# Kernel tuning notes

Measured on AMD Instinct MI355X. Metric: run time of the kernel, lower is better.

The kernel has to match this reference:

```python
import jax, jax.numpy as jnp
import numpy as np

WEIGHT = 1.0  # init kwarg: loss weight
N = 4096
D_FEAT = 128


def _pairwise_dist(x):
    # x: [n, d] -> D: [n, n] Euclidean distances (safe sqrt for grad at 0)
    sq = jnp.sum(x * x, axis=-1)
    d2 = sq[:, None] + sq[None, :] - 2.0 * (x @ x.T)
    d2 = jnp.maximum(d2, 0.0)
    pos = d2 > 1e-12
    return jnp.where(pos, jnp.sqrt(jnp.where(pos, d2, 1.0)), 0.0)


def _prim_mst(D):
    # Vectorized Prim: returns (parents, children) of the n-1 MST edges.
    # filtration value (VR complex truncated at max_dimension=1).
    n = D.shape[0]
    INF = jnp.finfo(D.dtype).max
    visited0 = jnp.zeros(n, dtype=bool).at[0].set(True)
    mind0 = D[0]
    parent0 = jnp.zeros(n, dtype=jnp.int32)

    def step(carry, _):
        visited, mind, parent = carry
        j = jnp.argmin(jnp.where(visited, INF, mind))
        pj = parent[j]
        visited = visited.at[j].set(True)
        better = (D[j] < mind) & (~visited)
        mind = jnp.where(better, D[j], mind)
        parent = jnp.where(better, j, parent)
        return (visited, mind, parent), (pj, j.astype(jnp.int32))

    _, (pjs, js) = jax.lax.scan(step, (visited0, mind0, parent0), None, length=n - 1)
    return pjs, js


def _h1_persistence(x):
    # H1 diagram for VR complex with max_dimension=1: a 1-cycle is born when a
    # non-MST edge appears; with no 2-simplices it never dies, so deaths are
    # capped at the maximal filtration value. Persistence = cap - birth.
    n = x.shape[0]
    D = _pairwise_dist(x)
    pjs, js = _prim_mst(D)
    tree = jnp.zeros((n, n), dtype=bool)
    tree = tree.at[pjs, js].set(True)
    tree = tree | tree.T
    iu = np.triu_indices(n, 1)  # static indices
    births = D[iu]              # [n*(n-1)/2]
    is_tree = tree[iu]
    cap = jnp.max(D)
    # tree edges are H0 (not H1): give them zero persistence (diagonal points)
    return jnp.where(is_tree, 0.0, cap - births)


def _wasserstein_1d(p1, p2):
    # 1-Wasserstein between equal-size persistence multisets via sorted matching
    # (deaths share a common cap per diagram, so matching by sorted persistence).
    return jnp.sum(jnp.abs(jnp.sort(p1) - jnp.sort(p2)))


def setup_inputs() -> dict:
    key = jax.random.key(0)
    k1, k2, k3, k4 = jax.random.split(key, 4)
    return {
        "graph1_features": jax.random.normal(k1, (N, D_FEAT), dtype=jnp.float32),
        "graph1_edges": jax.random.randint(k2, (2, 8 * N), 0, N, dtype=jnp.int64),
        "graph2_features": jax.random.normal(k3, (N, D_FEAT), dtype=jnp.float32),
        "graph2_edges": jax.random.randint(k4, (2, 8 * N), 0, N, dtype=jnp.int64),
    }


def reference(graph1_features, graph1_edges, graph2_features, graph2_edges):
    # edge tensors are unused: the torch forward builds VR complexes from the
    # point clouds only (build_from_points), matching the original module.
    p1 = _h1_persistence(graph1_features)
    p2 = _h1_persistence(graph2_features)
    return WEIGHT * _wasserstein_1d(p1, p2)
```

## Files before the change

### kernel.cpp

```cpp
#include <hip/hip_runtime.h>
#include <stdint.h>

#define NN 4096
#define DF 128
#define NBINS 16384
#define NSLAB 256
#define BORUVKA_ROUNDS 12

typedef __attribute__((ext_vector_type(8))) short short8;
typedef __attribute__((ext_vector_type(4))) float floatx4;
typedef __attribute__((ext_vector_type(4))) unsigned short ushort4_t;
typedef __attribute__((ext_vector_type(8))) unsigned short ushort8_t;
typedef __attribute__((ext_vector_type(4))) int int4_t;
typedef __attribute__((ext_vector_type(2))) unsigned uvec2;

__device__ __forceinline__ unsigned bin_of(float v, float scale) {
  if (v < 0.f) v = 0.f;
  unsigned b = (unsigned)(v * scale);
  return b >= (unsigned)NBINS ? (unsigned)(NBINS - 1) : b;
}

__device__ __forceinline__ void gload16(const unsigned short* g, unsigned short* l) {
  __builtin_amdgcn_global_load_lds(
      (const __attribute__((address_space(1))) void*)g,
      (__attribute__((address_space(3))) void*)l, 16, 0, 0);
}

__global__ void k_rownorm(const float* __restrict__ x1, const float* __restrict__ x2,
                          float* __restrict__ sq) {
  int i = blockIdx.x * blockDim.x + threadIdx.x;
  if (i >= 2 * NN) return;
  const float* x = (i < NN) ? x1 : x2;
  int r = i & (NN - 1);
  const float* row = x + (size_t)r * DF;
  float s = 0.f;
  for (int k = 0; k < DF; ++k) s += row[k] * row[k];
  sq[i] = s;
}

__global__ __launch_bounds__(256) void k_bound(const float* __restrict__ sq,
                                               float* __restrict__ hdrf) {
  int t = threadIdx.x;
  float m = 0.f;
  for (int i = t; i < 2 * NN; i += 256) m = fmaxf(m, sq[i]);
  for (int off = 32; off > 0; off >>= 1) m = fmaxf(m, __shfl_down(m, off, 64));
  __shared__ float wm[4];
  if ((t & 63) == 0) wm[t >> 6] = m;
  __syncthreads();
  if (t == 0) {
    float mm = fmaxf(fmaxf(wm[0], wm[1]), fmaxf(wm[2], wm[3]));
    float dbound = 2.f * sqrtf(mm);
    hdrf[2] = 65535.f / dbound;
    hdrf[3] = dbound / 65535.f;
  }
}

__global__ void k_split(const float* __restrict__ x1, const float* __restrict__ x2,
                        unsigned short* __restrict__ xh, unsigned short* __restrict__ xl) {
  int i = blockIdx.x * blockDim.x + threadIdx.x;
  if (i >= 2 * NN * DF) return;
  const float* x = (i < NN * DF) ? x1 : x2;
  float v = x[i & (NN * DF - 1)];
  unsigned u = __float_as_uint(v);
  unsigned hu = u & 0xffff0000u;
  float hf = __uint_as_float(hu);
  float lf = v - hf;
  unsigned lu = __float_as_uint(lf) & 0xffff0000u;
  xh[i] = (unsigned short)(hu >> 16);
  xl[i] = (unsigned short)(lu >> 16);
}

__global__ void k_binit(int* __restrict__ comp, unsigned long long* __restrict__ compbest,
                        unsigned long long* __restrict__ bestkey,
                        int* __restrict__ mstcnt, int* __restrict__ ncomp) {
  int i = blockIdx.x * blockDim.x + threadIdx.x;
  if (i >= 2 * NN) return;
  comp[i] = i & (NN - 1);
  compbest[i] = ~0ull;
  bestkey[i] = ~0ull;
  if ((i & (NN - 1)) == 0) {
    mstcnt[i >> 12] = 0;
    ncomp[i >> 12] = NN;
  }
}

#define SJ 136
__global__ __launch_bounds__(256) void k_dist(const unsigned short* __restrict__ Xhi,
                                              const unsigned short* __restrict__ Xlo,
                                              const float* __restrict__ sq,
                                              const float* __restrict__ hdrf,
                                              unsigned short* __restrict__ Qbase,
                                              unsigned long long* __restrict__ bestkey_base,
                                              unsigned* __restrict__ caps) {
  int bi = blockIdx.y, bj = blockIdx.x;
  if (bi > bj) return;
  bool offdiag = (bi != bj);
  int g = blockIdx.z;
  const unsigned short* xh = Xhi + (size_t)g * NN * DF;
  const unsigned short* xl = Xlo + (size_t)g * NN * DF;
  const float* sqg = sq + g * NN;
  unsigned short* Q = Qbase + (size_t)g * NN * NN;
  float qs = hdrf[2];
  int t = threadIdx.x;
  int w = t >> 6, lane = t & 63;
  int m = lane & 15, quad = lane >> 4;
  int iw = (w >> 1) * 64, jw = (w & 1) * 64;
  int i0 = bi * 128 + iw;
  int j0 = bj * 128 + jw;

  __shared__ __align__(16) unsigned short SB[128 * SJ];

  int baseRow = (w < 2) ? bi * 128 : bj * 128;
  const unsigned short* src = (w == 0 || w == 2) ? xh : xl;
  unsigned short* ldsPiece = &SB[w * 4096];
  int rsub = lane >> 2;
  int kpart = (lane & 3) ^ ((lane >> 3) & 3);
  int fr = (quad ^ ((m >> 1) & 3)) << 3;

  floatx4 acc[4][4];
#pragma unroll
  for (int ti = 0; ti < 4; ++ti)
#pragma unroll
    for (int tj = 0; tj < 4; ++tj) acc[ti][tj] = (floatx4){0.f, 0.f, 0.f, 0.f};

  for (int s = 0; s < 4; ++s) {
    int kc = s * 32;
    if (s) __syncthreads();
#pragma unroll
    for (int i = 0; i < 8; ++i) {
      const unsigned short* gp =
          src + (size_t)(baseRow + i * 16 + rsub) * DF + kc + kpart * 8;
      gload16(gp, &ldsPiece[i * 512]);
    }
    __syncthreads();
    short8 ah[4], al[4], bh[4], bl[4];
#pragma unroll
    for (int ti = 0; ti < 4; ++ti) {
      int ra = (iw + ti * 16 + m) * 32 + fr;
      int rb = (jw + ti * 16 + m) * 32 + fr;
      ah[ti] = *(const short8*)&SB[ra];
      al[ti] = *(const short8*)&SB[4096 + ra];
      bh[ti] = *(const short8*)&SB[8192 + rb];
      bl[ti] = *(const short8*)&SB[12288 + rb];
    }
#pragma unroll
    for (int ti = 0; ti < 4; ++ti)
#pragma unroll
      for (int tj = 0; tj < 4; ++tj) {
        acc[ti][tj] = __builtin_amdgcn_mfma_f32_16x16x32_bf16(ah[ti], bh[tj], acc[ti][tj], 0, 0, 0);
        acc[ti][tj] = __builtin_amdgcn_mfma_f32_16x16x32_bf16(ah[ti], bl[tj], acc[ti][tj], 0, 0, 0);
        acc[ti][tj] = __builtin_amdgcn_mfma_f32_16x16x32_bf16(al[ti], bh[tj], acc[ti][tj], 0, 0, 0);
      }
  }

  float sqj[4];
#pragma unroll
  for (int tj = 0; tj < 4; ++tj) sqj[tj] = sqg[j0 + tj * 16 + m];
  float mx = 0.f;
  ushort4_t qv[4][4];
#pragma unroll
  for (int ti = 0; ti < 4; ++ti) {
    int ib = i0 + ti * 16 + quad * 4;
    float sqiv[4];
#pragma unroll
    for (int r = 0; r < 4; ++r) sqiv[r] = sqg[ib + r];
#pragma unroll
    for (int tj = 0; tj < 4; ++tj) {
#pragma unroll
      for (int r = 0; r < 4; ++r) {
        float d2 = sqiv[r] + sqj[tj] - 2.f * acc[ti][tj][r];
        d2 = fmaxf(d2, 0.f);
        float d = (d2 > 1e-12f) ? sqrtf(d2) : 0.f;
        mx = fmaxf(mx, d);
        unsigned q = (unsigned)(d * qs + 0.5f);
        if (q > 65535u) q = 65535u;
        qv[ti][tj][r] = (unsigned short)q;
      }
    }
  }

  __syncthreads();
  unsigned short* T = SB;
  int sub = t >> 4, l16 = t & 15;
  int l31 = lane & 31, half = lane >> 5;
  unsigned long long* bkp = bestkey_base + (size_t)g * NN;

  auto prefill_rows = [&](int rbase, int cbase, bool exdiag) {
#pragma unroll 4
    for (int ii = 0; ii < 16; ++ii) {
      int rr = w * 32 + ii * 2 + half;
      uvec2 vv = *(const uvec2*)&T[rr * SJ + l31 * 4];
      int row = rbase + rr;
      unsigned qq[4] = {vv[0] & 0xffffu, vv[0] >> 16, vv[1] & 0xffffu, vv[1] >> 16};
      unsigned kmin = 0xffffffffu;
#pragma unroll
      for (int u = 0; u < 4; ++u) {
        int cl = l31 * 4 + u;
        if (!exdiag || (cbase + cl) != row) {
          unsigned key = (qq[u] << 7) | (unsigned)cl;
          if (key < kmin) kmin = key;
        }
      }
#pragma unroll
      for (int off2 = 1; off2 < 32; off2 <<= 1) {
        unsigned o = (unsigned)__shfl_xor((int)kmin, off2, 32);
        if (o < kmin) kmin = o;
      }
      if (l31 == 0 && kmin != 0xffffffffu) {
        unsigned qk = kmin >> 7, cl = kmin & 127u;
        unsigned long long key64 = ((unsigned long long)qk << 24) |
                                   ((unsigned long long)row << 12) |
                                   (unsigned)(cbase + cl);
        atomicMin(&bkp[row], key64);
      }
    }
  };

#pragma unroll
  for (int ti = 0; ti < 4; ++ti) {
    int il = iw + ti * 16 + quad * 4;
#pragma unroll
    for (int tj = 0; tj < 4; ++tj) {
      int jl = jw + tj * 16 + m;
      *(ushort4_t*)&T[jl * SJ + il] = qv[ti][tj];
    }
  }
  __syncthreads();
#pragma unroll
  for (int k = 0; k < 8; ++k) {
    int jl = k * 16 + sub;
    int4_t v = *(const int4_t*)&T[jl * SJ + l16 * 8];
    *(int4_t*)&Q[(size_t)(bj * 128 + jl) * NN + bi * 128 + l16 * 8] = v;
  }
  prefill_rows(bj * 128, bi * 128, !offdiag);

  if (offdiag) {
    __syncthreads();
#pragma unroll
    for (int ti = 0; ti < 4; ++ti) {
      int il = iw + ti * 16 + quad * 4;
#pragma unroll
      for (int tj = 0; tj < 4; ++tj) {
        int jl = jw + tj * 16 + m;
#pragma unroll
        for (int r = 0; r < 4; ++r) T[(il + r) * SJ + jl] = qv[ti][tj][r];
      }
    }
    __syncthreads();
#pragma unroll
    for (int k = 0; k < 8; ++k) {
      int il = k * 16 + sub;
      int4_t v = *(const int4_t*)&T[il * SJ + l16 * 8];
      *(int4_t*)&Q[(size_t)(bi * 128 + il) * NN + bj * 128 + l16 * 8] = v;
    }
    prefill_rows(bi * 128, bj * 128, false);
  }

  for (int off = 32; off > 0; off >>= 1) mx = fmaxf(mx, __shfl_down(mx, off, 64));
  __shared__ float wmax[4];
  if (lane == 0) wmax[w] = mx;
  __syncthreads();
  if (t == 0) {
    float mm = fmaxf(fmaxf(wmax[0], wmax[1]), fmaxf(wmax[2], wmax[3]));
    atomicMax(&caps[g], __float_as_uint(mm));
  }
}

__global__ __launch_bounds__(256) void k_minedge(const unsigned short* __restrict__ Qbase,
                                                 const int* __restrict__ comp_base,
                                                 unsigned long long* __restrict__ compbest_base,
                                                 unsigned long long* __restrict__ bestkey_base,
                                                 const int* __restrict__ ncomp) {
  int g = blockIdx.y;
  if (ncomp[g] == 1) return;
  int w = threadIdx.x >> 6, lane = threadIdx.x & 63;
  int v = blockIdx.x * 4 + w;
  const int* comp = comp_base + g * NN;
  unsigned long long* cbest = compbest_base + (size_t)g * NN;
  unsigned long long* bkp = bestkey_base + (size_t)g * NN;
  int cv = comp[v];
  unsigned long long bk = bkp[v];
  if (bk != ~0ull) {
    int bj = (int)(bk & 0xfffull);
    if (comp[bj] != cv) {
      if (lane == 0) atomicMin(&cbest[cv], bk);
      return;
    }
  }
  const unsigned short* row = Qbase + ((size_t)g * NN + (size_t)v) * NN;
  unsigned best = 0xffffffffu;
#pragma unroll 4
  for (int it = 0; it < NN / 256; ++it) {
    int jb = (it * 64 + lane) * 4;
    ushort4_t rw = *(const ushort4_t*)&row[jb];
    int4_t cj = *(const int4_t*)&comp[jb];
#pragma unroll
    for (int u = 0; u < 4; ++u) {
      if (cj[u] != cv) {
        unsigned key = ((unsigned)rw[u] << 12) | (unsigned)(jb + u);
        if (key < best) best = key;
      }
    }
  }
  for (int off = 32; off > 0; off >>= 1) {
    unsigned o = (unsigned)__shfl_down((int)best, off, 64);
    if (o < best) best = o;
  }
  if (lane == 0) {
    unsigned long long b64 = ~0ull;
    if (best != 0xffffffffu)
      b64 = ((unsigned long long)(best >> 12) << 24) |
            ((unsigned long long)v << 12) | (best & 0xfffu);
    bkp[v] = b64;
    if (b64 != ~0ull) atomicMin(&cbest[cv], b64);
  }
}

__global__ __launch_bounds__(1024) void k_hook(unsigned long long* __restrict__ compbest_base,
                                               int* __restrict__ comp_base,
                                               const float* __restrict__ hdrf,
                                               float* __restrict__ mstw_base,
                                               int* __restrict__ mstcnt,
                                               int* __restrict__ ncomp) {
  int g = blockIdx.x;
  if (ncomp[g] == 1) return;
  unsigned long long* cb = compbest_base + (size_t)g * NN;
  int* comp = comp_base + g * NN;
  float* mstw = mstw_base + g * (NN - 1);
  float qinv = hdrf[3];
  __shared__ int par[NN];
  __shared__ unsigned char live[NN];
  __shared__ int newcnt;
  int t = threadIdx.x;
  if (t == 0) newcnt = 0;
  for (int c = t; c < NN; c += 1024) {
    unsigned long long key = cb[c];
    bool a = (key != ~0ull);
    live[c] = a ? 1 : 0;
    int p = c;
    if (a) {
      int j = (int)(key & 0xfffull);
      p = comp[j];
    }
    par[c] = p;
  }
  __syncthreads();
  for (int c = t; c < NN; c += 1024) {
    int p = par[c];
    if (p != c && par[p] == c && c < p) par[c] = c;
  }
  __syncthreads();
  for (int c = t; c < NN; c += 1024) {
    if (live[c] && par[c] != c) {
      float w = (float)((unsigned)(cb[c] >> 24)) * qinv;
      int slot = atomicAdd(&mstcnt[g], 1);
      mstw[slot] = w;
    }
  }
  __syncthreads();
  for (;;) {
    int np[NN / 1024];
    bool ch = false;
    int k = 0;
    for (int c = t; c < NN; c += 1024, ++k) {
      int p = par[c];
      int pp = par[p];
      np[k] = pp;
      if (pp != p) ch = true;
    }
    __syncthreads();
    k = 0;
    for (int c = t; c < NN; c += 1024, ++k) par[c] = np[k];
    if (!__syncthreads_or(ch)) break;
  }
  int cnt = 0;
  for (int c = t; c < NN; c += 1024)
    if (live[c] && par[c] == c) cnt++;
  for (int off = 32; off > 0; off >>= 1) cnt += __shfl_down(cnt, off, 64);
  if ((t & 63) == 0 && cnt) atomicAdd(&newcnt, cnt);
  for (int v = t; v < NN; v += 1024) comp[v] = par[comp[v]];
  for (int c = t; c < NN; c += 1024) cb[c] = ~0ull;
  __syncthreads();
  if (t == 0) ncomp[g] = newcnt;
}

__global__ __launch_bounds__(256) void k_hist(const unsigned short* __restrict__ Qbase,
                                              const unsigned* __restrict__ caps,
                                              const float* __restrict__ hdrf,
                                              unsigned* __restrict__ Hs) {
  __shared__ unsigned h[NBINS];
  int t = threadIdx.x;
  for (int i = t; i < NBINS; i += 256) h[i] = 0;
  int b = blockIdx.x;
  int g = b >> 8, s = b & (NSLAB - 1);
  const unsigned short* Q = Qbase + (size_t)g * NN * NN;
  float cap = __uint_as_float(caps[g]);
  float capmax = fmaxf(__uint_as_float(caps[0]), __uint_as_float(caps[1]));
  float scale = (float)NBINS / capmax;
  float qinv = hdrf[3];
  __syncthreads();
  for (int p = s; p < NN / 2; p += NSLAB) {
#pragma unroll
    for (int half = 0; half < 2; ++half) {
      int rrow = half ? (NN - 1 - p) : p;
      const unsigned short* row = Q + (size_t)rrow * NN;
      int j0 = rrow + 1;
      int ja = (j0 + 7) & ~7;
      if (t < ja - j0)
        atomicAdd(&h[bin_of(cap - (float)row[j0 + t] * qinv, scale)], 1u);
      int nch = (NN - ja) >> 3;
      for (int c = t; c < nch; c += 256) {
        ushort8_t v8 = *(const ushort8_t*)&row[ja + c * 8];
#pragma unroll
        for (int u = 0; u < 8; ++u)
          atomicAdd(&h[bin_of(cap - (float)v8[u] * qinv, scale)], 1u);
      }
    }
  }
  __syncthreads();
  unsigned* slab = Hs + (size_t)b * NBINS;
  for (int i = t; i < NBINS; i += 256) slab[i] = h[i];
}

__global__ void k_treefix(const float* __restrict__ twbase, const unsigned* __restrict__ caps,
                          unsigned* __restrict__ Hs) {
  int g = blockIdx.y;
  unsigned* hist = Hs + (size_t)(g * NSLAB) * NBINS;
  float cap = __uint_as_float(caps[g]);
  float capmax = fmaxf(__uint_as_float(caps[0]), __uint_as_float(caps[1]));
  float scale = (float)NBINS / capmax;
  int idx = blockIdx.x * blockDim.x + threadIdx.x;
  if (idx < NN - 1) {
    float w = twbase[g * (NN - 1) + idx];
    atomicSub(&hist[bin_of(cap - w, scale)], 1u);
    atomicAdd(&hist[0], 1u);
  }
}

__global__ __launch_bounds__(256) void k_merge(const unsigned* __restrict__ Hs,
                                               unsigned* __restrict__ Hm) {
  int id = blockIdx.x * 256 + threadIdx.x;
  int g = id >> 14;
  int i = id & (NBINS - 1);
  const unsigned* base = Hs + (size_t)(g * NSLAB) * NBINS + i;
  unsigned sum = 0;
  for (int s = 0; s < NSLAB; ++s) sum += base[(size_t)s * NBINS];
  Hm[id] = sum;
}

__global__ __launch_bounds__(256) void k_w1(const unsigned* __restrict__ Hm,
                                            const unsigned* __restrict__ caps,
                                            float* __restrict__ out) {
  int t = threadIdx.x;
  const int PB = NBINS / 256;
  int base = t * PB;
  long long tsum = 0;
  for (int i = 0; i < PB; ++i)
    tsum += (long long)(int)(Hm[base + i] - Hm[NBINS + base + i]);
  int lane = t & 63, wid = t >> 6;
  long long incl = tsum;
  for (int off = 1; off < 64; off <<= 1) {
    long long o = __shfl_up(incl, off, 64);
    if (lane >= off) incl += o;
  }
  __shared__ long long wtot[4];
  if (lane == 63) wtot[wid] = incl;
  __syncthreads();
  long long run = incl - tsum;
  for (int w = 0; w < wid; ++w) run += wtot[w];
  unsigned long long local = 0;
  for (int i = 0; i < PB; ++i) {
    run += (long long)(int)(Hm[base + i] - Hm[NBINS + base + i]);
    local += (unsigned long long)(run < 0 ? -run : run);
  }
  for (int off = 32; off > 0; off >>= 1) local += __shfl_down(local, off, 64);
  __shared__ unsigned long long wl[4];
  if (lane == 0) wl[wid] = local;
  __syncthreads();
  if (t == 0) {
    float capmax = fmaxf(__uint_as_float(caps[0]), __uint_as_float(caps[1]));
    double dt = (double)capmax / (double)NBINS;
    out[0] = (float)((double)(wl[0] + wl[1] + wl[2] + wl[3]) * dt);
  }
}

__global__ void k_fail(float* out) { out[0] = -1234567.0f; }

extern "C" void kernel_launch(void* const* d_in, const int* in_sizes, int n_in,
                              void* d_out, int out_size, void* d_ws, size_t ws_size,
                              hipStream_t stream) {
  const float* x1 = (const float*)d_in[0];
  const float* x2 = (const float*)d_in[2];
  float* out = (float*)d_out;
  char* ws = (char*)d_ws;

  const size_t offQ = 0;
  const size_t offS = 2ull * NN * NN * 2ull;
  const size_t offHm = offS + 2ull * NSLAB * NBINS * 4ull;
  const size_t offHdr = offHm + 2ull * NBINS * 4ull;
  const size_t offSq = offHdr + 64;
  const size_t offTw = offSq + 2ull * NN * 4ull;
  const size_t offCb = (offTw + 2ull * (NN - 1) * 4ull + 7ull) & ~7ull;
  const size_t offBk = offCb + 2ull * NN * 8ull;
  const size_t offCp = offBk + 2ull * NN * 8ull;
  const size_t offMeta = offCp + 2ull * NN * 4ull;
  const size_t needed = offMeta + 64;
  if (ws_size < needed) {
    hipLaunchKernelGGL(k_fail, dim3(1), dim3(1), 0, stream, out);
    return;
  }

  unsigned short* Qbase = (unsigned short*)(ws + offQ);
  unsigned* Hs = (unsigned*)(ws + offS);
  unsigned short* Xhi = (unsigned short*)(ws + offS);
  unsigned short* Xlo = (unsigned short*)(ws + offS + 2ull * NN * DF * 2ull);
  unsigned* Hm = (unsigned*)(ws + offHm);
  unsigned* caps = (unsigned*)(ws + offHdr);
  float* hdrf = (float*)(ws + offHdr);
  float* sq = (float*)(ws + offSq);
  float* tw = (float*)(ws + offTw);
  unsigned long long* compbest = (unsigned long long*)(ws + offCb);
  unsigned long long* bestkey = (unsigned long long*)(ws + offBk);
  int* comp = (int*)(ws + offCp);
  int* mstcnt = (int*)(ws + offMeta);
  int* ncomp = (int*)(ws + offMeta + 8);

  hipMemsetAsync(ws + offHdr, 0, 64, stream);

  hipLaunchKernelGGL(k_rownorm, dim3((2 * NN + 255) / 256), dim3(256), 0, stream, x1, x2, sq);
  hipLaunchKernelGGL(k_bound, dim3(1), dim3(256), 0, stream, sq, hdrf);
  hipLaunchKernelGGL(k_split, dim3((2 * NN * DF + 255) / 256), dim3(256), 0, stream,
                     x1, x2, Xhi, Xlo);
  hipLaunchKernelGGL(k_binit, dim3((2 * NN + 255) / 256), dim3(256), 0, stream,
                     comp, compbest, bestkey, mstcnt, ncomp);
  hipLaunchKernelGGL(k_dist, dim3(NN / 128, NN / 128, 2), dim3(256), 0, stream,
                     Xhi, Xlo, sq, hdrf, Qbase, bestkey, caps);
  for (int r = 0; r < BORUVKA_ROUNDS; ++r) {
    hipLaunchKernelGGL(k_minedge, dim3(NN / 4, 2), dim3(256), 0, stream,
                       Qbase, comp, compbest, bestkey, ncomp);
    hipLaunchKernelGGL(k_hook, dim3(2), dim3(1024), 0, stream,
                       compbest, comp, hdrf, tw, mstcnt, ncomp);
  }
  hipLaunchKernelGGL(k_hist, dim3(2 * NSLAB), dim3(256), 0, stream, Qbase, caps, hdrf, Hs);
  hipLaunchKernelGGL(k_treefix, dim3(16, 2), dim3(256), 0, stream, tw, caps, Hs);
  hipLaunchKernelGGL(k_merge, dim3(2 * NBINS / 256), dim3(256), 0, stream, Hs, Hm);
  hipLaunchKernelGGL(k_w1, dim3(1), dim3(256), 0, stream, Hm, caps, out);
}
```

Measured before the change: 354.3 us.

## Replace per-row best-edge cache with per-segment minima for Boruvka min-edge search

The distance kernel now stores, for each row, the minimum quantized key of each 128-column segment (32 per row) instead of a single atomic row minimum. The min-edge kernel reads these 32 segment minima, takes the best among segments whose argmin lies outside the vertex's component, and rescans only those segments whose cached minimum is smaller but falls inside the component. This is meant to avoid full 4096-column row rescans in later Boruvka rounds. In exchange it adds a 1 MB segmin buffer plus per-segment stores in k_dist, and uses a serial loop over flagged segments.

```diff
diff --git a/kernel.cpp b/kernel.cpp
--- a/kernel.cpp
+++ b/kernel.cpp
@@ -13,6 +13,7 @@
 typedef __attribute__((ext_vector_type(8))) unsigned short ushort8_t;
 typedef __attribute__((ext_vector_type(4))) int int4_t;
 typedef __attribute__((ext_vector_type(2))) unsigned uvec2;
+typedef __attribute__((ext_vector_type(2))) int ivec2;
 
 __device__ __forceinline__ unsigned bin_of(float v, float scale) {
   if (v < 0.f) v = 0.f;
@@ -71,13 +72,11 @@
 }
 
 __global__ void k_binit(int* __restrict__ comp, unsigned long long* __restrict__ compbest,
-                        unsigned long long* __restrict__ bestkey,
                         int* __restrict__ mstcnt, int* __restrict__ ncomp) {
   int i = blockIdx.x * blockDim.x + threadIdx.x;
   if (i >= 2 * NN) return;
   comp[i] = i & (NN - 1);
   compbest[i] = ~0ull;
-  bestkey[i] = ~0ull;
   if ((i & (NN - 1)) == 0) {
     mstcnt[i >> 12] = 0;
     ncomp[i >> 12] = NN;
@@ -90,7 +89,7 @@
                                               const float* __restrict__ sq,
                                               const float* __restrict__ hdrf,
                                               unsigned short* __restrict__ Qbase,
-                                              unsigned long long* __restrict__ bestkey_base,
+                                              unsigned* __restrict__ segmin_base,
                                               unsigned* __restrict__ caps) {
   int bi = blockIdx.y, bj = blockIdx.x;
   if (bi > bj) return;
@@ -100,6 +99,7 @@
   const unsigned short* xl = Xlo + (size_t)g * NN * DF;
   const float* sqg = sq + g * NN;
   unsigned short* Q = Qbase + (size_t)g * NN * NN;
+  unsigned* smg = segmin_base + (size_t)g * NN * 32;
   float qs = hdrf[2];
   int t = threadIdx.x;
   int w = t >> 6, lane = t & 63;
@@ -183,9 +183,8 @@
   unsigned short* T = SB;
   int sub = t >> 4, l16 = t & 15;
   int l31 = lane & 31, half = lane >> 5;
-  unsigned long long* bkp = bestkey_base + (size_t)g * NN;
-
-  auto prefill_rows = [&](int rbase, int cbase, bool exdiag) {
+
+  auto prefill_rows = [&](int rbase, int cbase, int segidx, bool exdiag) {
 #pragma unroll 4
     for (int ii = 0; ii < 16; ++ii) {
       int rr = w * 32 + ii * 2 + half;
@@ -206,13 +205,7 @@
         unsigned o = (unsigned)__shfl_xor((int)kmin, off2, 32);
         if (o < kmin) kmin = o;
       }
-      if (l31 == 0 && kmin != 0xffffffffu) {
-        unsigned qk = kmin >> 7, cl = kmin & 127u;
-        unsigned long long key64 = ((unsigned long long)qk << 24) |
-                                   ((unsigned long long)row << 12) |
-                                   (unsigned)(cbase + cl);
-        atomicMin(&bkp[row], key64);
-      }
+      if (l31 == 0) smg[(size_t)row * 32 + segidx] = kmin;
     }
   };
 
@@ -232,7 +225,7 @@
     int4_t v = *(const int4_t*)&T[jl * SJ + l16 * 8];
     *(int4_t*)&Q[(size_t)(bj * 128 + jl) * NN + bi * 128 + l16 * 8] = v;
   }
-  prefill_rows(bj * 128, bi * 128, !offdiag);
+  prefill_rows(bj * 128, bi * 128, bi, !offdiag);
 
   if (offdiag) {
     __syncthreads();
@@ -253,7 +246,7 @@
       int4_t v = *(const int4_t*)&T[il * SJ + l16 * 8];
       *(int4_t*)&Q[(size_t)(bi * 128 + il) * NN + bj * 128 + l16 * 8] = v;
     }
-    prefill_rows(bi * 128, bj * 128, false);
+    prefill_rows(bi * 128, bj * 128, bj, false);
   }
 
   for (int off = 32; off > 0; off >>= 1) mx = fmaxf(mx, __shfl_down(mx, off, 64));
@@ -267,9 +260,9 @@
 }
 
 __global__ __launch_bounds__(256) void k_minedge(const unsigned short* __restrict__ Qbase,
+                                                 const unsigned* __restrict__ segmin_base,
                                                  const int* __restrict__ comp_base,
                                                  unsigned long long* __restrict__ compbest_base,
-                                                 unsigned long long* __restrict__ bestkey_base,
                                                  const int* __restrict__ ncomp) {
   int g = blockIdx.y;
   if (ncomp[g] == 1) return;
@@ -277,42 +270,50 @@
   int v = blockIdx.x * 4 + w;
   const int* comp = comp_base + g * NN;
   unsigned long long* cbest = compbest_base + (size_t)g * NN;
-  unsigned long long* bkp = bestkey_base + (size_t)g * NN;
   int cv = comp[v];
-  unsigned long long bk = bkp[v];
-  if (bk != ~0ull) {
-    int bj = (int)(bk & 0xfffull);
-    if (comp[bj] != cv) {
-      if (lane == 0) atomicMin(&cbest[cv], bk);
-      return;
-    }
-  }
-  const unsigned short* row = Qbase + ((size_t)g * NN + (size_t)v) * NN;
-  unsigned best = 0xffffffffu;
-#pragma unroll 4
-  for (int it = 0; it < NN / 256; ++it) {
-    int jb = (it * 64 + lane) * 4;
-    ushort4_t rw = *(const ushort4_t*)&row[jb];
-    int4_t cj = *(const int4_t*)&comp[jb];
-#pragma unroll
-    for (int u = 0; u < 4; ++u) {
-      if (cj[u] != cv) {
-        unsigned key = ((unsigned)rw[u] << 12) | (unsigned)(jb + u);
-        if (key < best) best = key;
-      }
-    }
-  }
-  for (int off = 32; off > 0; off >>= 1) {
-    unsigned o = (unsigned)__shfl_down((int)best, off, 64);
-    if (o < best) best = o;
-  }
-  if (lane == 0) {
-    unsigned long long b64 = ~0ull;
-    if (best != 0xffffffffu)
-      b64 = ((unsigned long long)(best >> 12) << 24) |
-            ((unsigned long long)v << 12) | (best & 0xfffu);
-    bkp[v] = b64;
-    if (b64 != ~0ull) atomicMin(&cbest[cv], b64);
+  const unsigned* sm = segmin_base + ((size_t)g * NN + (size_t)v) * 32;
+
+  unsigned key28 = 0xffffffffu;
+  bool incomp = false;
+  if (lane < 32) {
+    unsigned k23 = sm[lane];
+    unsigned q = k23 >> 7, cl = k23 & 127u;
+    unsigned col = (unsigned)lane * 128u + cl;
+    key28 = (q << 12) | col;
+    incomp = (comp[col] == cv);
+  }
+  unsigned a = (lane < 32 && !incomp) ? key28 : 0xffffffffu;
+#pragma unroll
+  for (int off = 1; off < 64; off <<= 1) {
+    unsigned o = (unsigned)__shfl_xor((int)a, off, 64);
+    if (o < a) a = o;
+  }
+  unsigned best = a;
+
+  unsigned long long flags = __ballot(lane < 32 && incomp && key28 < best);
+  if (flags) {
+    const unsigned short* row = Qbase + ((size_t)g * NN + (size_t)v) * NN;
+    while (flags) {
+      int s = (int)(__ffsll((long long)flags) - 1);
+      flags &= flags - 1;
+      int j = s * 128 + (lane << 1);
+      unsigned pq = *(const unsigned*)&row[j];
+      ivec2 cj = *(const ivec2*)&comp[j];
+      unsigned k1 = (cj[0] != cv) ? ((pq & 0xffffu) << 12) | (unsigned)j : 0xffffffffu;
+      unsigned k2 = (cj[1] != cv) ? ((pq >> 16) << 12) | (unsigned)(j + 1) : 0xffffffffu;
+      unsigned kk = k1 < k2 ? k1 : k2;
+#pragma unroll
+      for (int off = 1; off < 64; off <<= 1) {
+        unsigned o = (unsigned)__shfl_xor((int)kk, off, 64);
+        if (o < kk) kk = o;
+      }
+      if (kk < best) best = kk;
+    }
+  }
+  if (lane == 0 && best != 0xffffffffu) {
+    unsigned long long b64 = ((unsigned long long)(best >> 12) << 24) |
+                             ((unsigned long long)v << 12) | (best & 0xfffu);
+    atomicMin(&cbest[cv], b64);
   }
 }
 
@@ -501,8 +502,8 @@
   const size_t offSq = offHdr + 64;
   const size_t offTw = offSq + 2ull * NN * 4ull;
   const size_t offCb = (offTw + 2ull * (NN - 1) * 4ull + 7ull) & ~7ull;
-  const size_t offBk = offCb + 2ull * NN * 8ull;
-  const size_t offCp = offBk + 2ull * NN * 8ull;
+  const size_t offSeg = offCb + 2ull * NN * 8ull;
+  const size_t offCp = offSeg + 2ull * NN * 32ull * 4ull;
   const size_t offMeta = offCp + 2ull * NN * 4ull;
   const size_t needed = offMeta + 64;
   if (ws_size < needed) {
@@ -520,7 +521,7 @@
   float* sq = (float*)(ws + offSq);
   float* tw = (float*)(ws + offTw);
   unsigned long long* compbest = (unsigned long long*)(ws + offCb);
-  unsigned long long* bestkey = (unsigned long long*)(ws + offBk);
+  unsigned* segmin = (unsigned*)(ws + offSeg);
   int* comp = (int*)(ws + offCp);
   int* mstcnt = (int*)(ws + offMeta);
   int* ncomp = (int*)(ws + offMeta + 8);
@@ -532,12 +533,12 @@
   hipLaunchKernelGGL(k_split, dim3((2 * NN * DF + 255) / 256), dim3(256), 0, stream,
                      x1, x2, Xhi, Xlo);
   hipLaunchKernelGGL(k_binit, dim3((2 * NN + 255) / 256), dim3(256), 0, stream,
-                     comp, compbest, bestkey, mstcnt, ncomp);
+                     comp, compbest, mstcnt, ncomp);
   hipLaunchKernelGGL(k_dist, dim3(NN / 128, NN / 128, 2), dim3(256), 0, stream,
-                     Xhi, Xlo, sq, hdrf, Qbase, bestkey, caps);
+                     Xhi, Xlo, sq, hdrf, Qbase, segmin, caps);
   for (int r = 0; r < BORUVKA_ROUNDS; ++r) {
     hipLaunchKernelGGL(k_minedge, dim3(NN / 4, 2), dim3(256), 0, stream,
-                       Qbase, comp, compbest, bestkey, ncomp);
+                       Qbase, segmin, comp, compbest, ncomp);
     hipLaunchKernelGGL(k_hook, dim3(2), dim3(1024), 0, stream,
                        compbest, comp, hdrf, tw, mstcnt, ncomp);
   }
```

Result: no change. 349.5 us (-1.4%).
